# Optimization experiments

Measured on AMD Instinct MI355X. Metric: run time of the kernel, lower is better.

## Reference

```python
import jax, jax.numpy as jnp
import numpy as np

DN = ('NCDHW', 'OIDHW', 'NCDHW')

def conv3d(x, w, stride, padding):
    return jax.lax.conv_general_dilated(x, w, window_strides=stride, padding=padding, dimension_numbers=DN)

def swish(v):
    return v * jax.nn.sigmoid(v)

def setup_inputs() -> dict:
    key = jax.random.key(0)
    ks = jax.random.split(key, 16)
    B, Cin, Cout, E, D, H, W = 4, 64, 128, 256, 8, 128, 128
    r = lambda k, shp, s=0.05: jax.random.normal(k, shp, dtype=jnp.float32) * s
    return {
        'x': jax.random.normal(ks[0], (B, Cin, D, H, W), dtype=jnp.float32),
        'embed': jax.random.normal(ks[1], (B, E), dtype=jnp.float32),
        'context': jax.random.normal(ks[2], (B, E), dtype=jnp.float32),
        'w20': r(ks[3], (Cout, Cin, 3, 3, 3)),
        'b20': r(ks[4], (Cout,)),
        'w21': r(ks[5], (Cout, Cout, 3, 3, 3)),
        'd1_w': r(ks[6], (E, Cin)),
        'd1_b': r(ks[7], (Cin,)),
        'd2_w': r(ks[8], (E, Cout)),
        'd2_b': r(ks[9], (Cout,)),
        'res_w': r(ks[10], (Cout, Cin, 1, 1, 1)),
        'res_b': r(ks[11], (Cout,)),
        'down_w': r(ks[12], (Cout, Cout, 3, 3, 3)),
        'down_b': r(ks[13], (Cout,)),
    }

def reference(x, embed, context, w20, b20, w21, d1_w, d1_b, d2_w, d2_b, res_w, res_b, down_w, down_b):
    # --- ResBlockModulateBEST ---
    s1 = embed @ d1_w + d1_b                       # (B, Cin) time-embedding shift
    h = swish(x + s1[:, :, None, None, None])
    # dropout is identity in eval/reference mode
    h = conv3d(h, w20, (1, 1, 1), [(1, 1), (1, 1), (1, 1)]) + b20[None, :, None, None, None]
    h = swish(h)
    # modulated_conv3d: s scales the IN-channel axis of w21 per sample; since conv is
    # linear in its input channels this equals conv3d(h * s, w21) — same math, no
    # per-sample grouped conv needed.
    s2 = context @ d2_w + d2_b                     # (B, Cout == Cin of conv21)
    h = conv3d(h * s2[:, :, None, None, None], w21, (1, 1, 1), [(1, 1), (1, 1), (1, 1)])
    res = conv3d(x, res_w, (1, 1, 1), [(0, 0), (0, 0), (0, 0)]) + res_b[None, :, None, None, None]
    h = h + res
    # --- down path ---
    h = swish(h)
    out = conv3d(h, down_w, (1, 2, 2), [(1, 1), (0, 0), (0, 0)]) + down_b[None, :, None, None, None]
    return out  # (B, Cout, D, (H-3)//2+1, (W-3)//2+1) = (4,128,8,63,63)
```

## Files before the change

kernel.cpp:

```cpp
#include <hip/hip_runtime.h>
#include <cstdint>
#include <cstddef>

typedef __attribute__((ext_vector_type(8))) short bf16x8;
typedef __attribute__((ext_vector_type(4))) short bf16x4v;
typedef __attribute__((ext_vector_type(4))) float f32x4;

__device__ inline short f2bf(float f) {
  union { float f; unsigned u; } c; c.f = f;
  unsigned u = c.u;
  unsigned r = (u + 0x7fffu + ((u >> 16) & 1u)) >> 16;
  return (short)r;
}
__device__ inline float swish_f(float v) { return v / (1.f + __expf(-v)); }

__device__ inline void gld_lds16(const void* g, void* l) {
  __builtin_amdgcn_global_load_lds((const __attribute__((address_space(1))) void*)g,
                                   (__attribute__((address_space(3))) void*)l, 16, 0, 0);
}

#define ACQ(VM) do {                                                     \
    asm volatile("s_waitcnt vmcnt(" VM ")" ::: "memory");                \
    __builtin_amdgcn_s_barrier();                                        \
    asm volatile("" ::: "memory");                                       \
  } while (0)
#define REL() do {                                                       \
    asm volatile("" ::: "memory");                                       \
    __builtin_amdgcn_s_barrier();                                        \
  } while (0)

__global__ __launch_bounds__(256) void scales_kernel(
    const float* __restrict__ embed, const float* __restrict__ context,
    const float* __restrict__ d1w, const float* __restrict__ d1b,
    const float* __restrict__ d2w, const float* __restrict__ d2b,
    float* __restrict__ s1, float* __restrict__ s2) {
  int tid = blockIdx.x * 256 + threadIdx.x;
  if (tid < 256) {
    int b = tid >> 6, c = tid & 63;
    float acc = d1b[c];
    for (int e = 0; e < 256; ++e) acc += embed[b * 256 + e] * d1w[e * 64 + c];
    s1[tid] = acc;
  } else if (tid < 768) {
    int o = tid - 256;
    int b = o >> 7, c = o & 127;
    float acc = d2b[c];
    for (int e = 0; e < 256; ++e) acc += context[b * 256 + e] * d2w[e * 128 + c];
    s2[o] = acc;
  }
}

__global__ __launch_bounds__(256) void prep_w_kernel(
    const float* __restrict__ w20, const float* __restrict__ w21,
    const float* __restrict__ wdn, const float* __restrict__ rsw,
    short* __restrict__ wt20, short* __restrict__ wt21,
    short* __restrict__ wtdn, short* __restrict__ rw) {
  for (int o = blockIdx.x * 256 + threadIdx.x; o < 1114112; o += gridDim.x * 256) {
    if (o < 221184) {
      int t = o >> 13, rem = o & 8191, co = rem >> 6, ci = rem & 63;
      wt20[o] = f2bf(w20[(co * 64 + ci) * 27 + t]);
    } else if (o < 663552) {
      int p = o - 221184;
      int t = p >> 14, rem = p & 16383, co = rem >> 7, ci = rem & 127;
      wt21[p] = f2bf(w21[(co * 128 + ci) * 27 + t]);
    } else if (o < 1105920) {
      int p = o - 663552;
      int t = p >> 14, rem = p & 16383, co = rem >> 7, ci = rem & 127;
      wtdn[p] = f2bf(wdn[(co * 128 + ci) * 27 + t]);
    } else {
      int p = o - 1105920;
      rw[p] = f2bf(rsw[p]);
    }
  }
}

__global__ __launch_bounds__(256) void prep_h1_kernel(
    const float* __restrict__ xin, const float* __restrict__ s1,
    short* __restrict__ h1) {
  __shared__ __align__(16) short sm[128 * 72];
  const int tid = threadIdx.x;
  const int gid = blockIdx.x;
  const int y = gid & 127, z = (gid >> 7) & 7, b = gid >> 10;
  const float* xbase = xin + (size_t)b * 8388608 + (size_t)z * 16384 + (size_t)y * 128;
#pragma unroll
  for (int i = 0; i < 8; ++i) {
    int e = i * 256 + tid;
    int ci = e >> 5, x4 = e & 31;
    float4 v = *(const float4*)(xbase + (size_t)ci * 131072 + x4 * 4);
    float s = s1[b * 64 + ci];
    sm[(x4 * 4 + 0) * 72 + ci] = f2bf(swish_f(v.x + s));
    sm[(x4 * 4 + 1) * 72 + ci] = f2bf(swish_f(v.y + s));
    sm[(x4 * 4 + 2) * 72 + ci] = f2bf(swish_f(v.z + s));
    sm[(x4 * 4 + 3) * 72 + ci] = f2bf(swish_f(v.w + s));
  }
  __syncthreads();
  short* orow = h1 + (size_t)gid * 8192;
#pragma unroll
  for (int i = 0; i < 4; ++i) {
    int e = i * 256 + tid;
    int xx = e >> 3, c8 = e & 7;
    *(bf16x8*)(orow + e * 8) = *(const bf16x8*)(&sm[xx * 72 + c8 * 8]);
  }
}

__global__ __launch_bounds__(256, 3) void conv20_kernel(
    const short* __restrict__ h1, const short* __restrict__ wt,
    const float* __restrict__ b20, const float* __restrict__ s2,
    short* __restrict__ h2) {
  __shared__ __align__(16) short sm[24704];
  const int tid = threadIdx.x;
  const int bi = blockIdx.x;
  const int xcd = bi & 7, slot = bi >> 3;
  const int yo = slot & 15, z = (slot >> 4) & 7, b = slot >> 7;
  const int y = xcd * 16 + yo;
  const int gid = b * 1024 + z * 128 + y;
  const int lane = tid & 63, wave = tid >> 6;
  const int wm = wave >> 1, wn = wave & 1;
  const int q = lane >> 4, n0 = lane & 15;
  const bf16x8 zz = {0, 0, 0, 0, 0, 0, 0, 0};
  short* inbuf = sm;
  f32x4 acc[4][4];
#pragma unroll
  for (int i = 0; i < 4; ++i)
#pragma unroll
    for (int j = 0; j < 4; ++j) acc[i][j] = (f32x4){0.f, 0.f, 0.f, 0.f};

  auto wstage = [&](int s) {
    const short* src = wt + (s << 13);
    short* dst = sm + 8320 + ((s & 1) << 13);
    int r = lane >> 3, ss = lane & 7;
#pragma unroll
    for (int i = 0; i < 4; ++i) {
      int c = wave * 4 + i;
      gld_lds16(src + ((c * 8 + r) << 6) + ((ss ^ r) << 3), dst + (c << 9));
    }
  };
  auto instage = [&](int it) {
    int kz = it / 3, ky = it - kz * 3;
    int zi = z + kz - 1, yi = y + ky - 1;
    if (zi >= 0 && zi < 8 && yi >= 0 && yi < 128) {
      const short* row = h1 + ((size_t)(b * 1024 + zi * 128 + yi) << 13);
#pragma unroll
      for (int i = 0; i < 4; ++i) {
        int x0 = 1 + 8 * (wave * 4 + i);
        int x = x0 + (lane >> 3);
        int c8 = (lane & 7) ^ (x & 7);
        gld_lds16(row + ((x - 1) << 6) + (c8 << 3), inbuf + (x0 << 6));
      }
    } else {
#pragma unroll
      for (int i = 0; i < 4; ++i)
        *(bf16x8*)(&inbuf[64 + (i * 256 + tid) * 8]) = zz;
      asm volatile("s_waitcnt lgkmcnt(0)" ::: "memory");
    }
  };

  if (tid < 16) {
    int hf = tid >> 3, u = tid & 7;
    *(bf16x8*)(&inbuf[(hf ? 129 : 0) * 64 + u * 8]) = zz;
  }
  wstage(0);
  instage(0);
  __syncthreads();

  for (int s = 0; s < 27; ++s) {
    const int it3 = s / 3, kx = s - it3 * 3;
    if (s < 26) wstage(s + 1);
    if (s < 26) ACQ("4"); else ACQ("0");
    const short* w = sm + 8320 + ((s & 1) << 13);
#pragma unroll
    for (int ch = 0; ch < 2; ++ch) {
      bf16x8 af[4], bb[4];
#pragma unroll
      for (int i = 0; i < 4; ++i)
        af[i] = *(const bf16x8*)(&w[(wm * 64 + i * 16 + n0) * 64 + (((ch * 4 + q) ^ (n0 & 7)) << 3)]);
#pragma unroll
      for (int j = 0; j < 4; ++j) {
        int xx = wn * 64 + j * 16 + n0 + kx;
        bb[j] = *(const bf16x8*)(&inbuf[xx * 64 + (((ch * 4 + q) ^ (xx & 7)) << 3)]);
      }
#pragma unroll
      for (int i = 0; i < 4; ++i)
#pragma unroll
        for (int j = 0; j < 4; ++j)
          acc[i][j] = __builtin_amdgcn_mfma_f32_16x16x32_bf16(af[i], bb[j], acc[i][j], 0, 0, 0);
    }
    REL();
    if (kx == 2 && it3 < 8) instage(it3 + 1);
  }
#pragma unroll
  for (int i = 0; i < 4; ++i) {
    const int mb = wm * 64 + i * 16 + q * 4;
    const float4 bias = *(const float4*)(b20 + mb);
    const float4 sc = *(const float4*)(s2 + b * 128 + mb);
#pragma unroll
    for (int j = 0; j < 4; ++j) {
      const int n = wn * 64 + j * 16 + n0;
      bf16x4v pk;
      pk.x = f2bf(swish_f(acc[i][j][0] + bias.x) * sc.x);
      pk.y = f2bf(swish_f(acc[i][j][1] + bias.y) * sc.y);
      pk.z = f2bf(swish_f(acc[i][j][2] + bias.z) * sc.z);
      pk.w = f2bf(swish_f(acc[i][j][3] + bias.w) * sc.w);
      *(bf16x4v*)(&sm[n * 136 + mb]) = pk;
    }
  }
  __syncthreads();
  short* orow = h2 + (size_t)gid * 16384;
#pragma unroll
  for (int i = 0; i < 8; ++i) {
    int e = i * 256 + tid;
    int xx = e >> 4, c8 = e & 15;
    *(bf16x8*)(orow + e * 8) = *(const bf16x8*)(&sm[xx * 136 + c8 * 8]);
  }
}

__global__ __launch_bounds__(256, 2) void conv21_kernel(
    const short* __restrict__ h2, const short* __restrict__ wt,
    const float* __restrict__ xin, const short* __restrict__ rw,
    const float* __restrict__ res_b, short* __restrict__ h3) {
  __shared__ __align__(16) short sm[33024];
  const int tid = threadIdx.x;
  const int bi = blockIdx.x;
  const int xcd = bi & 7, slot = bi >> 3;
  const int yo = slot & 15, z = (slot >> 4) & 7, b = slot >> 7;
  const int y = xcd * 16 + yo;
  const int gid = b * 1024 + z * 128 + y;
  const int lane = tid & 63, wave = tid >> 6;
  const int wm = wave >> 1, wn = wave & 1;
  const int q = lane >> 4, n0 = lane & 15;
  const bf16x8 zz = {0, 0, 0, 0, 0, 0, 0, 0};
  short* inbuf = sm;
  f32x4 acc[4][4];
#pragma unroll
  for (int i = 0; i < 4; ++i)
#pragma unroll
    for (int j = 0; j < 4; ++j) acc[i][j] = (f32x4){0.f, 0.f, 0.f, 0.f};

  auto wstage = [&](int s) {
    int it6 = s / 6, sub = s - it6 * 6, kx = sub >> 1, ch2 = sub & 1;
    const short* src = wt + (((it6 * 3 + kx) << 14) + (ch2 << 6));
    short* dst = sm + 16640 + ((s & 1) << 13);
    int r = lane >> 3, ss = lane & 7;
#pragma unroll
    for (int i = 0; i < 4; ++i) {
      int c = wave * 4 + i;
      gld_lds16(src + ((c * 8 + r) << 7) + ((ss ^ r) << 3), dst + (c << 9));
    }
  };
  auto instage = [&](int it) {
    int kz = it / 3, ky = it - kz * 3;
    int zi = z + kz - 1, yi = y + ky - 1;
    if (zi >= 0 && zi < 8 && yi >= 0 && yi < 128) {
      const short* row = h2 + ((size_t)(b * 1024 + zi * 128 + yi) << 14);
#pragma unroll
      for (int i = 0; i < 8; ++i) {
        int x0 = 1 + 4 * (wave * 8 + i);
        int x = x0 + (lane >> 4);
        int c8 = (lane & 15) ^ (x & 15);
        gld_lds16(row + ((x - 1) << 7) + (c8 << 3), inbuf + (x0 << 7));
      }
    } else {
#pragma unroll
      for (int i = 0; i < 8; ++i)
        *(bf16x8*)(&inbuf[128 + (i * 256 + tid) * 8]) = zz;
      asm volatile("s_waitcnt lgkmcnt(0)" ::: "memory");
    }
  };

  if (tid < 32) {
    int hf = tid >> 4, u = tid & 15;
    *(bf16x8*)(&inbuf[(hf ? 129 : 0) * 128 + u * 8]) = zz;
  }
  wstage(0);
  instage(0);
  __syncthreads();

  float4 xv[8];
  for (int s = 0; s < 54; ++s) {
    const int it6 = s / 6, sub = s - it6 * 6, kx = sub >> 1, ch2 = sub & 1;
    if (s < 53) wstage(s + 1);
    if (s == 52)      ACQ("12");
    else if (s == 53) ACQ("0");
    else              ACQ("4");
    if (s == 51) {
      const float* xb = xin + (size_t)b * 8388608 + (size_t)z * 16384 + (size_t)y * 128;
#pragma unroll
      for (int i = 0; i < 8; ++i) {
        int e = i * 256 + tid;
        int ci = e >> 5, x4 = e & 31;
        xv[i] = *(const float4*)(xb + (size_t)ci * 131072 + x4 * 4);
      }
    }
    const short* w = sm + 16640 + ((s & 1) << 13);
#pragma unroll
    for (int chL = 0; chL < 2; ++chL) {
      const int ch = ch2 * 2 + chL;
      bf16x8 af[4], bb[4];
#pragma unroll
      for (int i = 0; i < 4; ++i)
        af[i] = *(const bf16x8*)(&w[(wm * 64 + i * 16 + n0) * 64 + (((chL * 4 + q) ^ (n0 & 7)) << 3)]);
#pragma unroll
      for (int j = 0; j < 4; ++j) {
        int xx = wn * 64 + j * 16 + n0 + kx;
        bb[j] = *(const bf16x8*)(&inbuf[(xx << 7) + (((ch * 4 + q) ^ (xx & 15)) << 3)]);
      }
#pragma unroll
      for (int i = 0; i < 4; ++i)
#pragma unroll
        for (int j = 0; j < 4; ++j)
          acc[i][j] = __builtin_amdgcn_mfma_f32_16x16x32_bf16(af[i], bb[j], acc[i][j], 0, 0, 0);
    }
    REL();
    if (sub == 5 && it6 < 8) instage(it6 + 1);
  }
  short* rbuf = sm + 16640;
  {
#pragma unroll
    for (int i = 0; i < 8; ++i) {
      int e = i * 256 + tid;
      int ci = e >> 5, x4 = e & 31;
      int u0 = ci >> 3, cl = ci & 7;
#pragma unroll
      for (int k = 0; k < 4; ++k) {
        int xx = x4 * 4 + k;
        float fv = (k == 0) ? xv[i].x : (k == 1) ? xv[i].y : (k == 2) ? xv[i].z : xv[i].w;
        rbuf[xx * 64 + ((u0 ^ (xx & 7)) << 3) + cl] = f2bf(fv);
      }
    }
  }
  __syncthreads();
#pragma unroll
  for (int ch = 0; ch < 2; ++ch) {
    bf16x8 af[4], bb[4];
#pragma unroll
    for (int i = 0; i < 4; ++i)
      af[i] = *(const bf16x8*)(rw + (wm * 64 + i * 16 + n0) * 64 + ch * 32 + q * 8);
#pragma unroll
    for (int j = 0; j < 4; ++j) {
      int xx = wn * 64 + j * 16 + n0;
      bb[j] = *(const bf16x8*)(&rbuf[xx * 64 + (((ch * 4 + q) ^ (xx & 7)) << 3)]);
    }
#pragma unroll
    for (int i = 0; i < 4; ++i)
#pragma unroll
      for (int j = 0; j < 4; ++j)
        acc[i][j] = __builtin_amdgcn_mfma_f32_16x16x32_bf16(af[i], bb[j], acc[i][j], 0, 0, 0);
  }
  __syncthreads();
#pragma unroll
  for (int i = 0; i < 4; ++i) {
    const int mb = wm * 64 + i * 16 + q * 4;
    const float4 bias = *(const float4*)(res_b + mb);
#pragma unroll
    for (int j = 0; j < 4; ++j) {
      const int n = wn * 64 + j * 16 + n0;
      bf16x4v pk;
      pk.x = f2bf(swish_f(acc[i][j][0] + bias.x));
      pk.y = f2bf(swish_f(acc[i][j][1] + bias.y));
      pk.z = f2bf(swish_f(acc[i][j][2] + bias.z));
      pk.w = f2bf(swish_f(acc[i][j][3] + bias.w));
      *(bf16x4v*)(&sm[n * 136 + mb]) = pk;
    }
  }
  __syncthreads();
  short* orow = h3 + (size_t)gid * 16384;
#pragma unroll
  for (int i = 0; i < 8; ++i) {
    int e = i * 256 + tid;
    int xx = e >> 4, c8 = e & 15;
    *(bf16x8*)(orow + e * 8) = *(const bf16x8*)(&sm[xx * 136 + c8 * 8]);
  }
}

__global__ __launch_bounds__(256, 2) void down_kernel(
    const short* __restrict__ h3, const short* __restrict__ wt,
    const float* __restrict__ dnb, float* __restrict__ out) {
  __shared__ __align__(16) short sm[33024];
  const int tid = threadIdx.x;
  const int bi = blockIdx.x;
  const int o = (bi & 7) * 252 + (bi >> 3);
  const int yo = o % 63;
  const int zb = o / 63;
  const int z = zb & 7, b = zb >> 3;
  const int lane = tid & 63, wave = tid >> 6;
  const int wm = wave >> 1, wn = wave & 1;
  const int q = lane >> 4, n0 = lane & 15;
  const bf16x8 zz = {0, 0, 0, 0, 0, 0, 0, 0};
  short* inbuf = sm;
  f32x4 acc[4][2];
#pragma unroll
  for (int i = 0; i < 4; ++i)
#pragma unroll
    for (int j = 0; j < 2; ++j) acc[i][j] = (f32x4){0.f, 0.f, 0.f, 0.f};

  auto wstage = [&](int s) {
    int it6 = s / 6, sub = s - it6 * 6, kx = sub >> 1, ch2 = sub & 1;
    const short* src = wt + (((it6 * 3 + kx) << 14) + (ch2 << 6));
    short* dst = sm + 16640 + ((s & 1) << 13);
    int r = lane >> 3, ss = lane & 7;
#pragma unroll
    for (int i = 0; i < 4; ++i) {
      int c = wave * 4 + i;
      gld_lds16(src + ((c * 8 + r) << 7) + ((ss ^ r) << 3), dst + (c << 9));
    }
  };
  auto instage = [&](int it) {
    int kz = it / 3, ky = it - kz * 3;
    int zi = z + kz - 1;
    int yi = 2 * yo + ky;
    if (zi >= 0 && zi < 8) {
      const short* row = h3 + ((size_t)(b * 1024 + zi * 128 + yi) << 14);
#pragma unroll
      for (int i = 0; i < 8; ++i) {
        int x0 = 4 * (wave * 8 + i);
        int x = x0 + (lane >> 4);
        int c8 = (lane & 15) ^ (x & 15);
        gld_lds16(row + (x << 7) + (c8 << 3), inbuf + (x0 << 7));
      }
    } else {
#pragma unroll
      for (int i = 0; i < 8; ++i)
        *(bf16x8*)(&inbuf[(i * 256 + tid) * 8]) = zz;
      asm volatile("s_waitcnt lgkmcnt(0)" ::: "memory");
    }
  };

  if (tid < 32) {
    int hf = tid >> 4, u = tid & 15;
    *(bf16x8*)(&inbuf[(128 + hf) * 128 + u * 8]) = zz;
  }
  wstage(0);
  instage(0);
  __syncthreads();

  for (int s = 0; s < 54; ++s) {
    const int it6 = s / 6, sub = s - it6 * 6, kx = sub >> 1, ch2 = sub & 1;
    if (s < 53) wstage(s + 1);
    if (s < 53) ACQ("4"); else ACQ("0");
    const short* w = sm + 16640 + ((s & 1) << 13);
#pragma unroll
    for (int chL = 0; chL < 2; ++chL) {
      const int ch = ch2 * 2 + chL;
      bf16x8 af[4], bb[2];
#pragma unroll
      for (int i = 0; i < 4; ++i)
        af[i] = *(const bf16x8*)(&w[(wm * 64 + i * 16 + n0) * 64 + (((chL * 4 + q) ^ (n0 & 7)) << 3)]);
#pragma unroll
      for (int j = 0; j < 2; ++j) {
        int xp = 2 * (wn * 32 + j * 16 + n0) + kx;
        bb[j] = *(const bf16x8*)(&inbuf[(xp << 7) + (((ch * 4 + q) ^ (xp & 15)) << 3)]);
      }
#pragma unroll
      for (int i = 0; i < 4; ++i)
#pragma unroll
        for (int j = 0; j < 2; ++j)
          acc[i][j] = __builtin_amdgcn_mfma_f32_16x16x32_bf16(af[i], bb[j], acc[i][j], 0, 0, 0);
    }
    REL();
    if (sub == 5 && it6 < 8) instage(it6 + 1);
  }
  float* fsm = (float*)sm;
#pragma unroll
  for (int i = 0; i < 4; ++i) {
    const int mb = wm * 64 + i * 16 + q * 4;
    const float4 bias = *(const float4*)(dnb + mb);
#pragma unroll
    for (int j = 0; j < 2; ++j) {
      const int n = wn * 32 + j * 16 + n0;
      f32x4 v;
      v[0] = acc[i][j][0] + bias.x;
      v[1] = acc[i][j][1] + bias.y;
      v[2] = acc[i][j][2] + bias.z;
      v[3] = acc[i][j][3] + bias.w;
      *(f32x4*)(&fsm[n * 132 + mb]) = v;
    }
  }
  __syncthreads();
#pragma unroll
  for (int it = 0; it < 32; ++it) {
    int idx = it * 256 + tid;
    int co = idx >> 6, xl = idx & 63;
    if (xl < 63)
      out[((size_t)(b * 128 + co) * 8 + z) * 3969 + yo * 63 + xl] = fsm[xl * 132 + co];
  }
}

extern "C" void kernel_launch(void* const* d_in, const int* in_sizes, int n_in,
                              void* d_out, int out_size, void* d_ws, size_t ws_size,
                              hipStream_t stream) {
  const float* x       = (const float*)d_in[0];
  const float* embed   = (const float*)d_in[1];
  const float* context = (const float*)d_in[2];
  const float* w20     = (const float*)d_in[3];
  const float* b20     = (const float*)d_in[4];
  const float* w21     = (const float*)d_in[5];
  const float* d1w     = (const float*)d_in[6];
  const float* d1b     = (const float*)d_in[7];
  const float* d2w     = (const float*)d_in[8];
  const float* d2b     = (const float*)d_in[9];
  const float* resw    = (const float*)d_in[10];
  const float* resb    = (const float*)d_in[11];
  const float* dnw     = (const float*)d_in[12];
  const float* dnb     = (const float*)d_in[13];
  float* out = (float*)d_out;
  char* ws = (char*)d_ws;
  float* s1   = (float*)(ws + 0);
  float* s2   = (float*)(ws + 1024);
  short* wt20 = (short*)(ws + 4096);
  short* wt21 = (short*)(ws + 446464);
  short* wtdn = (short*)(ws + 1331200);
  short* rw   = (short*)(ws + 2215936);
  short* h1   = (short*)(ws + 2232320);
  short* h2   = (short*)(ws + 69341184);
  short* h3   = (short*)(ws + 203558912);

  scales_kernel<<<3, 256, 0, stream>>>(embed, context, d1w, d1b, d2w, d2b, s1, s2);
  prep_w_kernel<<<1088, 256, 0, stream>>>(w20, w21, dnw, resw, wt20, wt21, wtdn, rw);
  prep_h1_kernel<<<4096, 256, 0, stream>>>(x, s1, h1);
  conv20_kernel<<<4096, 256, 0, stream>>>(h1, wt20, b20, s2, h2);
  conv21_kernel<<<4096, 256, 0, stream>>>(h2, wt21, x, rw, resb, h3);
  down_kernel<<<2016, 256, 0, stream>>>(h3, wtdn, dnb, out);
}
```

Before: 1.055 ms.

## Software-pipeline LDS operand loads across conv stages with MFMA priority boost

```diff
diff --git a/kernel.cpp b/kernel.cpp
--- a/kernel.cpp
+++ b/kernel.cpp
@@ -162,31 +162,61 @@
   instage(0);
   __syncthreads();
 
-  for (int s = 0; s < 27; ++s) {
-    const int it3 = s / 3, kx = s - it3 * 3;
-    if (s < 26) wstage(s + 1);
-    if (s < 26) ACQ("4"); else ACQ("0");
-    const short* w = sm + 8320 + ((s & 1) << 13);
-#pragma unroll
-    for (int ch = 0; ch < 2; ++ch) {
-      bf16x8 af[4], bb[4];
-#pragma unroll
-      for (int i = 0; i < 4; ++i)
-        af[i] = *(const bf16x8*)(&w[(wm * 64 + i * 16 + n0) * 64 + (((ch * 4 + q) ^ (n0 & 7)) << 3)]);
-#pragma unroll
-      for (int j = 0; j < 4; ++j) {
-        int xx = wn * 64 + j * 16 + n0 + kx;
-        bb[j] = *(const bf16x8*)(&inbuf[xx * 64 + (((ch * 4 + q) ^ (xx & 7)) << 3)]);
-      }
-#pragma unroll
-      for (int i = 0; i < 4; ++i)
-#pragma unroll
-        for (int j = 0; j < 4; ++j)
-          acc[i][j] = __builtin_amdgcn_mfma_f32_16x16x32_bf16(af[i], bb[j], acc[i][j], 0, 0, 0);
-    }
+  bf16x8 af[2][4], bbA[2][4], bbB[2][4];
+
+#define C20_AF(PAR)                                                            \
+  { const short* w_ = sm + 8320 + ((PAR) << 13);                               \
+    _Pragma("unroll") for (int ch = 0; ch < 2; ++ch)                           \
+    _Pragma("unroll") for (int i = 0; i < 4; ++i)                              \
+      af[ch][i] = *(const bf16x8*)(&w_[(wm * 64 + i * 16 + n0) * 64 +          \
+                                       (((ch * 4 + q) ^ (n0 & 7)) << 3)]); }
+#define C20_BB(KX, BB)                                                         \
+  { _Pragma("unroll") for (int ch = 0; ch < 2; ++ch)                           \
+    _Pragma("unroll") for (int j = 0; j < 4; ++j) {                            \
+      int xx = wn * 64 + j * 16 + n0 + (KX);                                   \
+      BB[ch][j] = *(const bf16x8*)(&inbuf[xx * 64 +                            \
+                                          (((ch * 4 + q) ^ (xx & 7)) << 3)]); } }
+#define C20_MFMA(BB)                                                           \
+  { __builtin_amdgcn_s_setprio(1);                                             \
+    _Pragma("unroll") for (int ch = 0; ch < 2; ++ch)                           \
+    _Pragma("unroll") for (int i = 0; i < 4; ++i)                              \
+    _Pragma("unroll") for (int j = 0; j < 4; ++j)                              \
+      acc[i][j] = __builtin_amdgcn_mfma_f32_16x16x32_bf16(af[ch][i], BB[ch][j],\
+                                                          acc[i][j], 0, 0, 0); \
+    __builtin_amdgcn_s_setprio(0); }
+
+  for (int g = 0; g < 8; ++g) {
+    const int s3 = g * 3;
+    wstage(s3 + 1); ACQ("4");
+    C20_AF(g & 1);
+    C20_BB(0, bbA);
+    C20_BB(1, bbB);
+    C20_MFMA(bbA);
     REL();
-    if (kx == 2 && it3 < 8) instage(it3 + 1);
-  }
+    wstage(s3 + 2); ACQ("4");
+    C20_AF((g & 1) ^ 1);
+    C20_BB(2, bbA);
+    C20_MFMA(bbB);
+    REL();
+    wstage(s3 + 3); ACQ("4");
+    C20_AF(g & 1);
+    C20_MFMA(bbA);
+    REL();
+    instage(g + 1);
+  }
+  {
+    wstage(25); ACQ("4"); C20_AF(0);
+    C20_BB(0, bbA); C20_BB(1, bbB);
+    C20_MFMA(bbA); REL();
+    wstage(26); ACQ("4"); C20_AF(1);
+    C20_BB(2, bbA);
+    C20_MFMA(bbB); REL();
+    ACQ("0"); C20_AF(0);
+    C20_MFMA(bbA); REL();
+  }
+#undef C20_AF
+#undef C20_BB
+#undef C20_MFMA
 #pragma unroll
   for (int i = 0; i < 4; ++i) {
     const int mb = wm * 64 + i * 16 + q * 4;
@@ -274,14 +304,66 @@
   instage(0);
   __syncthreads();
 
+  bf16x8 af[2][4], bbA[2][4], bbB[2][4];
   float4 xv[8];
-  for (int s = 0; s < 54; ++s) {
-    const int it6 = s / 6, sub = s - it6 * 6, kx = sub >> 1, ch2 = sub & 1;
-    if (s < 53) wstage(s + 1);
-    if (s == 52)      ACQ("12");
-    else if (s == 53) ACQ("0");
-    else              ACQ("4");
-    if (s == 51) {
+
+#define C21_AF(PAR)                                                            \
+  { const short* w_ = sm + 16640 + ((PAR) << 13);                              \
+    _Pragma("unroll") for (int chL = 0; chL < 2; ++chL)                        \
+    _Pragma("unroll") for (int i = 0; i < 4; ++i)                              \
+      af[chL][i] = *(const bf16x8*)(&w_[(wm * 64 + i * 16 + n0) * 64 +         \
+                                        (((chL * 4 + q) ^ (n0 & 7)) << 3)]); }
+#define C21_BB(KX, CH2, BB)                                                    \
+  { _Pragma("unroll") for (int chL = 0; chL < 2; ++chL) {                      \
+      const int ch = (CH2) * 2 + chL;                                          \
+      _Pragma("unroll") for (int j = 0; j < 4; ++j) {                          \
+        int xx = wn * 64 + j * 16 + n0 + (KX);                                 \
+        BB[chL][j] = *(const bf16x8*)(&inbuf[(xx << 7) +                       \
+                                      (((ch * 4 + q) ^ (xx & 15)) << 3)]); } } }
+#define C21_MFMA(BB)                                                           \
+  { __builtin_amdgcn_s_setprio(1);                                             \
+    _Pragma("unroll") for (int chL = 0; chL < 2; ++chL)                        \
+    _Pragma("unroll") for (int i = 0; i < 4; ++i)                              \
+    _Pragma("unroll") for (int j = 0; j < 4; ++j)                              \
+      acc[i][j] = __builtin_amdgcn_mfma_f32_16x16x32_bf16(af[chL][i], BB[chL][j],\
+                                                          acc[i][j], 0, 0, 0); \
+    __builtin_amdgcn_s_setprio(0); }
+
+  for (int g = 0; g < 8; ++g) {
+    const int s6 = g * 6;
+    wstage(s6 + 1); ACQ("4");
+    C21_AF(0);
+    C21_BB(0, 0, bbA);
+    C21_BB(0, 1, bbB);
+    C21_MFMA(bbA); REL();
+    wstage(s6 + 2); ACQ("4"); C21_AF(1);
+    C21_BB(1, 0, bbA);
+    C21_MFMA(bbB); REL();
+    wstage(s6 + 3); ACQ("4"); C21_AF(0);
+    C21_BB(1, 1, bbB);
+    C21_MFMA(bbA); REL();
+    wstage(s6 + 4); ACQ("4"); C21_AF(1);
+    C21_BB(2, 0, bbA);
+    C21_MFMA(bbB); REL();
+    wstage(s6 + 5); ACQ("4"); C21_AF(0);
+    C21_BB(2, 1, bbB);
+    C21_MFMA(bbA); REL();
+    wstage(s6 + 6); ACQ("4"); C21_AF(1);
+    C21_MFMA(bbB); REL();
+    instage(g + 1);
+  }
+  {
+    wstage(49); ACQ("4"); C21_AF(0);
+    C21_BB(0, 0, bbA); C21_BB(0, 1, bbB);
+    C21_MFMA(bbA); REL();
+    wstage(50); ACQ("4"); C21_AF(1);
+    C21_BB(1, 0, bbA);
+    C21_MFMA(bbB); REL();
+    wstage(51); ACQ("4"); C21_AF(0);
+    C21_BB(1, 1, bbB);
+    C21_MFMA(bbA); REL();
+    wstage(52); ACQ("4");
+    {
       const float* xb = xin + (size_t)b * 8388608 + (size_t)z * 16384 + (size_t)y * 128;
 #pragma unroll
       for (int i = 0; i < 8; ++i) {
@@ -290,28 +372,20 @@
         xv[i] = *(const float4*)(xb + (size_t)ci * 131072 + x4 * 4);
       }
     }
-    const short* w = sm + 16640 + ((s & 1) << 13);
-#pragma unroll
-    for (int chL = 0; chL < 2; ++chL) {
-      const int ch = ch2 * 2 + chL;
-      bf16x8 af[4], bb[4];
-#pragma unroll
-      for (int i = 0; i < 4; ++i)
-        af[i] = *(const bf16x8*)(&w[(wm * 64 + i * 16 + n0) * 64 + (((chL * 4 + q) ^ (n0 & 7)) << 3)]);
-#pragma unroll
-      for (int j = 0; j < 4; ++j) {
-        int xx = wn * 64 + j * 16 + n0 + kx;
-        bb[j] = *(const bf16x8*)(&inbuf[(xx << 7) + (((ch * 4 + q) ^ (xx & 15)) << 3)]);
-      }
-#pragma unroll
-      for (int i = 0; i < 4; ++i)
-#pragma unroll
-        for (int j = 0; j < 4; ++j)
-          acc[i][j] = __builtin_amdgcn_mfma_f32_16x16x32_bf16(af[i], bb[j], acc[i][j], 0, 0, 0);
-    }
-    REL();
-    if (sub == 5 && it6 < 8) instage(it6 + 1);
-  }
+    C21_AF(1);
+    C21_BB(2, 0, bbA);
+    C21_MFMA(bbB); REL();
+    wstage(53); ACQ("12");
+    C21_AF(0);
+    C21_BB(2, 1, bbB);
+    C21_MFMA(bbA); REL();
+    ACQ("0");
+    C21_AF(1);
+    C21_MFMA(bbB); REL();
+  }
+#undef C21_AF
+#undef C21_BB
+#undef C21_MFMA
   short* rbuf = sm + 16640;
   {
 #pragma unroll
@@ -323,27 +397,27 @@
       for (int k = 0; k < 4; ++k) {
         int xx = x4 * 4 + k;
         float fv = (k == 0) ? xv[i].x : (k == 1) ? xv[i].y : (k == 2) ? xv[i].z : xv[i].w;
-        rbuf[xx * 64 + ((u0 ^ (xx & 7)) << 3) + cl] = f2bf(fv);
+        rbuf[xx * 64 + ((u0 ^ (xx & 7) ^ ((xx >> 3) & 7)) << 3) + cl] = f2bf(fv);
       }
     }
   }
   __syncthreads();
 #pragma unroll
   for (int ch = 0; ch < 2; ++ch) {
-    bf16x8 af[4], bb[4];
+    bf16x8 raf[4], rbb[4];
 #pragma unroll
     for (int i = 0; i < 4; ++i)
-      af[i] = *(const bf16x8*)(rw + (wm * 64 + i * 16 + n0) * 64 + ch * 32 + q * 8);
+      raf[i] = *(const bf16x8*)(rw + (wm * 64 + i * 16 + n0) * 64 + ch * 32 + q * 8);
 #pragma unroll
     for (int j = 0; j < 4; ++j) {
       int xx = wn * 64 + j * 16 + n0;
-      bb[j] = *(const bf16x8*)(&rbuf[xx * 64 + (((ch * 4 + q) ^ (xx & 7)) << 3)]);
+      rbb[j] = *(const bf16x8*)(&rbuf[xx * 64 + (((ch * 4 + q) ^ (xx & 7) ^ ((xx >> 3) & 7)) << 3)]);
     }
 #pragma unroll
     for (int i = 0; i < 4; ++i)
 #pragma unroll
       for (int j = 0; j < 4; ++j)
-        acc[i][j] = __builtin_amdgcn_mfma_f32_16x16x32_bf16(af[i], bb[j], acc[i][j], 0, 0, 0);
+        acc[i][j] = __builtin_amdgcn_mfma_f32_16x16x32_bf16(raf[i], rbb[j], acc[i][j], 0, 0, 0);
   }
   __syncthreads();
 #pragma unroll
@@ -432,32 +506,74 @@
   instage(0);
   __syncthreads();
 
-  for (int s = 0; s < 54; ++s) {
-    const int it6 = s / 6, sub = s - it6 * 6, kx = sub >> 1, ch2 = sub & 1;
-    if (s < 53) wstage(s + 1);
-    if (s < 53) ACQ("4"); else ACQ("0");
-    const short* w = sm + 16640 + ((s & 1) << 13);
-#pragma unroll
-    for (int chL = 0; chL < 2; ++chL) {
-      const int ch = ch2 * 2 + chL;
-      bf16x8 af[4], bb[2];
-#pragma unroll
-      for (int i = 0; i < 4; ++i)
-        af[i] = *(const bf16x8*)(&w[(wm * 64 + i * 16 + n0) * 64 + (((chL * 4 + q) ^ (n0 & 7)) << 3)]);
-#pragma unroll
-      for (int j = 0; j < 2; ++j) {
-        int xp = 2 * (wn * 32 + j * 16 + n0) + kx;
-        bb[j] = *(const bf16x8*)(&inbuf[(xp << 7) + (((ch * 4 + q) ^ (xp & 15)) << 3)]);
-      }
-#pragma unroll
-      for (int i = 0; i < 4; ++i)
-#pragma unroll
-        for (int j = 0; j < 2; ++j)
-          acc[i][j] = __builtin_amdgcn_mfma_f32_16x16x32_bf16(af[i], bb[j], acc[i][j], 0, 0, 0);
-    }
-    REL();
-    if (sub == 5 && it6 < 8) instage(it6 + 1);
-  }
+  bf16x8 af[2][4], bbA[2][2], bbB[2][2];
+
+#define DN_AF(PAR)                                                             \
+  { const short* w_ = sm + 16640 + ((PAR) << 13);                              \
+    _Pragma("unroll") for (int chL = 0; chL < 2; ++chL)                        \
+    _Pragma("unroll") for (int i = 0; i < 4; ++i)                              \
+      af[chL][i] = *(const bf16x8*)(&w_[(wm * 64 + i * 16 + n0) * 64 +         \
+                                        (((chL * 4 + q) ^ (n0 & 7)) << 3)]); }
+#define DN_BB(KX, CH2, BB)                                                     \
+  { _Pragma("unroll") for (int chL = 0; chL < 2; ++chL) {                      \
+      const int ch = (CH2) * 2 + chL;                                          \
+      _Pragma("unroll") for (int j = 0; j < 2; ++j) {                          \
+        int xp = 2 * (wn * 32 + j * 16 + n0) + (KX);                           \
+        BB[chL][j] = *(const bf16x8*)(&inbuf[(xp << 7) +                       \
+                                      (((ch * 4 + q) ^ (xp & 15)) << 3)]); } } }
+#define DN_MFMA(BB)                                                            \
+  { __builtin_amdgcn_s_setprio(1);                                             \
+    _Pragma("unroll") for (int chL = 0; chL < 2; ++chL)                        \
+    _Pragma("unroll") for (int i = 0; i < 4; ++i)                              \
+    _Pragma("unroll") for (int j = 0; j < 2; ++j)                              \
+      acc[i][j] = __builtin_amdgcn_mfma_f32_16x16x32_bf16(af[chL][i], BB[chL][j],\
+                                                          acc[i][j], 0, 0, 0); \
+    __builtin_amdgcn_s_setprio(0); }
+
+  for (int g = 0; g < 8; ++g) {
+    const int s6 = g * 6;
+    wstage(s6 + 1); ACQ("4"); DN_AF(0);
+    DN_BB(0, 0, bbA);
+    DN_BB(0, 1, bbB);
+    DN_MFMA(bbA); REL();
+    wstage(s6 + 2); ACQ("4"); DN_AF(1);
+    DN_BB(1, 0, bbA);
+    DN_MFMA(bbB); REL();
+    wstage(s6 + 3); ACQ("4"); DN_AF(0);
+    DN_BB(1, 1, bbB);
+    DN_MFMA(bbA); REL();
+    wstage(s6 + 4); ACQ("4"); DN_AF(1);
+    DN_BB(2, 0, bbA);
+    DN_MFMA(bbB); REL();
+    wstage(s6 + 5); ACQ("4"); DN_AF(0);
+    DN_BB(2, 1, bbB);
+    DN_MFMA(bbA); REL();
+    wstage(s6 + 6); ACQ("4"); DN_AF(1);
+    DN_MFMA(bbB); REL();
+    instage(g + 1);
+  }
+  {
+    wstage(49); ACQ("4"); DN_AF(0);
+    DN_BB(0, 0, bbA); DN_BB(0, 1, bbB);
+    DN_MFMA(bbA); REL();
+    wstage(50); ACQ("4"); DN_AF(1);
+    DN_BB(1, 0, bbA);
+    DN_MFMA(bbB); REL();
+    wstage(51); ACQ("4"); DN_AF(0);
+    DN_BB(1, 1, bbB);
+    DN_MFMA(bbA); REL();
+    wstage(52); ACQ("4"); DN_AF(1);
+    DN_BB(2, 0, bbA);
+    DN_MFMA(bbB); REL();
+    wstage(53); ACQ("4"); DN_AF(0);
+    DN_BB(2, 1, bbB);
+    DN_MFMA(bbA); REL();
+    ACQ("0"); DN_AF(1);
+    DN_MFMA(bbB); REL();
+  }
+#undef DN_AF
+#undef DN_BB
+#undef DN_MFMA
   float* fsm = (float*)sm;
 #pragma unroll
   for (int i = 0; i < 4; ++i) {
@@ -471,7 +587,7 @@
       v[1] = acc[i][j][1] + bias.y;
       v[2] = acc[i][j][2] + bias.z;
       v[3] = acc[i][j][3] + bias.w;
-      *(f32x4*)(&fsm[n * 132 + mb]) = v;
+      *(f32x4*)(&fsm[n * 133 + mb]) = v;
     }
   }
   __syncthreads();
@@ -480,7 +596,7 @@
     int idx = it * 256 + tid;
     int co = idx >> 6, xl = idx & 63;
     if (xl < 63)
-      out[((size_t)(b * 128 + co) * 8 + z) * 3969 + yo * 63 + xl] = fsm[xl * 132 + co];
+      out[((size_t)(b * 128 + co) * 8 + z) * 3969 + yo * 63 + xl] = fsm[xl * 133 + co];
   }
 }
 
```

Result: slower. 1.268 ms (+20.2%).
